# Kernel tuning notes

Measured on AMD Instinct MI355X. Metric: run time of the kernel, lower is better.

## Reference

```python
import jax, jax.numpy as jnp
import numpy as np

N, T, H, E = 16384, 4, 64, 262144
NEG_SLOPE = 0.2  # LeakyReLU slope for GAT-style attention
LN_EPS = 1e-5


def setup_inputs() -> dict:
    key = jax.random.key(0)
    ks = jax.random.split(key, 24)
    p = {}
    p["pred"] = jax.random.normal(ks[0], (N, T, H), jnp.float32)
    p["ei_structural"] = jax.random.randint(ks[1], (2, E), 0, N, jnp.int32)
    p["ei_functional"] = jax.random.randint(ks[2], (2, E), 0, N, jnp.int32)
    scale = 1.0 / np.sqrt(H)
    i = 3
    for l in range(2):
        for et in ("s", "f"):
            p[f"W{l}{et}"] = (jax.random.normal(ks[i], (H, H), jnp.float32) * scale); i += 1
            p[f"a{l}{et}"] = (jax.random.normal(ks[i], (H,), jnp.float32) * scale); i += 1
        p[f"g{l}"] = jnp.ones((H,), jnp.float32)
        p[f"b{l}"] = jnp.zeros((H,), jnp.float32)
    return p


def _conv(x, ei, W, a, n_dst):
    """Attention-based ST graph conv, temporal_kernel_size=1 (per-step)."""
    h = jnp.einsum('nth,hd->ntd', x, W)          # [N,T,H] linear transform
    src, dst = ei[0], ei[1]
    he = h[src]                                   # [E,T,H] gather per edge
    logits = jax.nn.leaky_relu(jnp.einsum('eth,h->et', he, a), NEG_SLOPE)
    m = jax.ops.segment_max(logits, dst, num_segments=n_dst)     # [N,T]
    ex = jnp.exp(logits - m[dst])                 # stable softmax over incoming edges
    den = jax.ops.segment_sum(ex, dst, num_segments=n_dst)
    alpha = ex / den[dst]                         # [E,T]
    return jax.ops.segment_sum(alpha[..., None] * he, dst, num_segments=n_dst)


def _ln(x, g, b):
    mu = x.mean(-1, keepdims=True)
    v = x.var(-1, keepdims=True)
    return (x - mu) * jax.lax.rsqrt(v + LN_EPS) * g + b


def reference(pred, ei_structural, ei_functional,
              W0s, a0s, W0f, a0f, g0, b0,
              W1s, a1s, W1f, a1f, g1, b1):
    x = pred
    layers = ((W0s, a0s, W0f, a0f, g0, b0), (W1s, a1s, W1f, a1f, g1, b1))
    for (Ws, av, Wf, af, g, b) in layers:
        ms = _conv(x, ei_structural, Ws, av, N)
        mf = _conv(x, ei_functional, Wf, af, N)
        # sum(messages)/len(messages), residual, LayerNorm over H (dropout=identity in eval)
        x = _ln(x + 0.5 * (ms + mf), g, b)
    return x
```

## Files before the change

kernel.cpp:

```cpp
#include <hip/hip_runtime.h>
#include <hip/hip_bf16.h>

#define NN 16384
#define TT 4
#define HH 64
#define NT (NN * TT)
#define NEG_SLOPE 0.2f
#define LN_EPS 1e-5f

typedef __attribute__((ext_vector_type(8))) short short8;
typedef __attribute__((ext_vector_type(4))) float f32x4;

__device__ __forceinline__ float bf2f(unsigned short u) {
    return __uint_as_float((unsigned)u << 16);
}
__device__ __forceinline__ unsigned short f2bf(float f) {
    unsigned u = __float_as_uint(f);
    return (unsigned short)((u + 0x7FFF + ((u >> 16) & 1)) >> 16);
}


__global__ void zero_kernel(int* __restrict__ a, int n) {
    int i = blockIdx.x * blockDim.x + threadIdx.x;
    if (i < n) a[i] = 0;
}

__global__ void hist2_kernel(const int* __restrict__ dst_s, const int* __restrict__ dst_f,
                             int* __restrict__ cnt2, int E) {
    int e = blockIdx.x * blockDim.x + threadIdx.x;
    if (e < E) {
        atomicAdd(&cnt2[dst_s[e]], 1);
    } else {
        e -= E;
        if (e < E) atomicAdd(&cnt2[NN + dst_f[e]], 1);
    }
}

__global__ __launch_bounds__(256) void scanA_kernel(const int* __restrict__ cnt2,
                                                    int* __restrict__ partial) {
    __shared__ int wsum[4];
    const int lane = threadIdx.x & 63;
    const int wv = threadIdx.x >> 6;
    int v = cnt2[blockIdx.x * 256 + threadIdx.x];
#pragma unroll
    for (int off = 32; off > 0; off >>= 1) v += __shfl_xor(v, off, 64);
    if (lane == 0) wsum[wv] = v;
    __syncthreads();
    if (threadIdx.x == 0)
        partial[blockIdx.x] = wsum[0] + wsum[1] + wsum[2] + wsum[3];
}

__global__ __launch_bounds__(128) void scanB_kernel(int* __restrict__ partial) {
    const int lane = threadIdx.x & 63;
    int v = partial[threadIdx.x];
    int inc = v;
#pragma unroll
    for (int off = 1; off < 64; off <<= 1) {
        int t = __shfl_up(inc, off, 64);
        if (lane >= off) inc += t;
    }
    partial[threadIdx.x] = inc - v;
}

__global__ __launch_bounds__(256) void scanC_kernel(const int* __restrict__ cnt2,
                                                    const int* __restrict__ partial,
                                                    int* __restrict__ rp2,
                                                    int* __restrict__ cur2) {
    __shared__ int wsum[4];
    const int lane = threadIdx.x & 63;
    const int wv = threadIdx.x >> 6;
    const int gidx = blockIdx.x * 256 + threadIdx.x;
    const int set = gidx >> 14;
    const int i = gidx & (NN - 1);
    int v = cnt2[gidx];
    int inc = v;
#pragma unroll
    for (int off = 1; off < 64; off <<= 1) {
        int t = __shfl_up(inc, off, 64);
        if (lane >= off) inc += t;
    }
    if (lane == 63) wsum[wv] = inc;
    __syncthreads();
    int wbase = 0;
#pragma unroll
    for (int w = 0; w < 4; w++)
        if (w < wv) wbase += wsum[w];
    int excl = (inc - v) + wbase + partial[blockIdx.x];
    int* rp = rp2 + set * (NN + 1);
    rp[i] = excl;
    cur2[gidx] = excl;
    if (i == NN - 1) rp[NN] = excl + v;
}

__global__ void scatter2_kernel(const int* __restrict__ ei_s, const int* __restrict__ ei_f,
                                int* __restrict__ cur2, int* __restrict__ col2, int E) {
    int e = blockIdx.x * blockDim.x + threadIdx.x;
    if (e < E) {
        int d = ei_s[E + e];
        int pos = atomicAdd(&cur2[d], 1);
        col2[pos] = ei_s[e];
    } else {
        e -= E;
        if (e < E) {
            int d = ei_f[E + e];
            int pos = atomicAdd(&cur2[NN + d], 1);
            col2[E + pos] = ei_f[e];
        }
    }
}


__global__ __launch_bounds__(256) void transform2_kernel(
    const float4* __restrict__ x4,
    const float* __restrict__ Ws, const float* __restrict__ as_,
    const float* __restrict__ Wf, const float* __restrict__ af,
    unsigned short* __restrict__ h_s, float* __restrict__ sc_s,
    unsigned short* __restrict__ h_f, float* __restrict__ sc_f) {
    const int lane = threadIdx.x & 63;
    const int wv = threadIdx.x >> 6;
    const int m = lane & 15;
    const int quad = lane >> 4;

    short8 Bs[4][2], Bf[4][2];
#pragma unroll
    for (int c = 0; c < 4; c++) {
#pragma unroll
        for (int ks = 0; ks < 2; ks++) {
#pragma unroll
            for (int j = 0; j < 8; j++) {
                int k = ks * 32 + quad * 8 + j;
                int n = c * 16 + m;
                Bs[c][ks][j] = (short)f2bf(Ws[k * 64 + n]);
                Bf[c][ks][j] = (short)f2bf(Wf[k * 64 + n]);
            }
        }
    }
    float a_s[4], a_f[4];
#pragma unroll
    for (int c = 0; c < 4; c++) { a_s[c] = as_[c * 16 + m]; a_f[c] = af[c * 16 + m]; }

    const int rowbase = blockIdx.x * 128 + wv * 32;
#pragma unroll
    for (int rt = 0; rt < 2; rt++) {
        const int row0 = rowbase + rt * 16;
        const long xbase = (long)(row0 + m) * 16 + quad * 2;
        float4 xa = x4[xbase];
        float4 xb = x4[xbase + 1];
        float4 xc = x4[xbase + 8];
        float4 xd = x4[xbase + 9];
        short8 A0, A1;
        A0[0] = (short)f2bf(xa.x); A0[1] = (short)f2bf(xa.y);
        A0[2] = (short)f2bf(xa.z); A0[3] = (short)f2bf(xa.w);
        A0[4] = (short)f2bf(xb.x); A0[5] = (short)f2bf(xb.y);
        A0[6] = (short)f2bf(xb.z); A0[7] = (short)f2bf(xb.w);
        A1[0] = (short)f2bf(xc.x); A1[1] = (short)f2bf(xc.y);
        A1[2] = (short)f2bf(xc.z); A1[3] = (short)f2bf(xc.w);
        A1[4] = (short)f2bf(xd.x); A1[5] = (short)f2bf(xd.y);
        A1[6] = (short)f2bf(xd.z); A1[7] = (short)f2bf(xd.w);

        f32x4 accs[4], accf[4];
#pragma unroll
        for (int c = 0; c < 4; c++) {
            accs[c] = (f32x4){0.f, 0.f, 0.f, 0.f};
            accf[c] = (f32x4){0.f, 0.f, 0.f, 0.f};
        }
#pragma unroll
        for (int c = 0; c < 4; c++) {
            accs[c] = __builtin_amdgcn_mfma_f32_16x16x32_bf16(A0, Bs[c][0], accs[c], 0, 0, 0);
            accs[c] = __builtin_amdgcn_mfma_f32_16x16x32_bf16(A1, Bs[c][1], accs[c], 0, 0, 0);
            accf[c] = __builtin_amdgcn_mfma_f32_16x16x32_bf16(A0, Bf[c][0], accf[c], 0, 0, 0);
            accf[c] = __builtin_amdgcn_mfma_f32_16x16x32_bf16(A1, Bf[c][1], accf[c], 0, 0, 0);
        }
#pragma unroll
        for (int reg = 0; reg < 4; reg++) {
            const int row = row0 + quad * 4 + reg;
            float ps = 0.f, pf = 0.f;
#pragma unroll
            for (int c = 0; c < 4; c++) {
                h_s[(long)row * 64 + c * 16 + m] = f2bf(accs[c][reg]);
                h_f[(long)row * 64 + c * 16 + m] = f2bf(accf[c][reg]);
                ps = fmaf(accs[c][reg], a_s[c], ps);
                pf = fmaf(accf[c][reg], a_f[c], pf);
            }
#pragma unroll
            for (int off = 1; off < 16; off <<= 1) {
                ps += __shfl_xor(ps, off, 64);
                pf += __shfl_xor(pf, off, 64);
            }
            if (m == 0) {
                sc_s[row] = (ps > 0.f) ? ps : NEG_SLOPE * ps;
                sc_f[row] = (pf > 0.f) ? pf : NEG_SLOPE * pf;
            }
        }
    }
}


__device__ __forceinline__ void agg_set(const ushort4* __restrict__ h4,
                                        const float* __restrict__ sc,
                                        const int* __restrict__ rp,
                                        const int* __restrict__ col,
                                        int n, int t, int lane, float4& msg) {
    const int beg = rp[n], end = rp[n + 1];
    float den = 0.f;
    float ax = 0.f, ay = 0.f, az = 0.f, aw = 0.f;
    int j = beg;
    for (; j + 8 <= end; j += 8) {
        int s[8];
        float l[8];
        ushort4 hh[8];
#pragma unroll
        for (int u = 0; u < 8; u++) s[u] = col[j + u];
#pragma unroll
        for (int u = 0; u < 8; u++) l[u] = sc[s[u] * 4 + t];
#pragma unroll
        for (int u = 0; u < 8; u++) hh[u] = h4[s[u] * 64 + lane];
#pragma unroll
        for (int u = 0; u < 8; u++) {
            float e = __expf(l[u]);
            den += e;
            ax = fmaf(e, bf2f(hh[u].x), ax);
            ay = fmaf(e, bf2f(hh[u].y), ay);
            az = fmaf(e, bf2f(hh[u].z), az);
            aw = fmaf(e, bf2f(hh[u].w), aw);
        }
    }
    for (; j + 4 <= end; j += 4) {
        int s[4];
        float l[4];
        ushort4 hh[4];
#pragma unroll
        for (int u = 0; u < 4; u++) s[u] = col[j + u];
#pragma unroll
        for (int u = 0; u < 4; u++) l[u] = sc[s[u] * 4 + t];
#pragma unroll
        for (int u = 0; u < 4; u++) hh[u] = h4[s[u] * 64 + lane];
#pragma unroll
        for (int u = 0; u < 4; u++) {
            float e = __expf(l[u]);
            den += e;
            ax = fmaf(e, bf2f(hh[u].x), ax);
            ay = fmaf(e, bf2f(hh[u].y), ay);
            az = fmaf(e, bf2f(hh[u].z), az);
            aw = fmaf(e, bf2f(hh[u].w), aw);
        }
    }
    for (; j < end; j++) {
        int s0 = col[j];
        float l0 = sc[s0 * 4 + t];
        ushort4 h0 = h4[s0 * 64 + lane];
        float e0 = __expf(l0);
        den += e0;
        ax = fmaf(e0, bf2f(h0.x), ax);
        ay = fmaf(e0, bf2f(h0.y), ay);
        az = fmaf(e0, bf2f(h0.z), az);
        aw = fmaf(e0, bf2f(h0.w), aw);
    }
    if (end > beg) {
        float r = 1.f / den;
        msg.x = ax * r; msg.y = ay * r; msg.z = az * r; msg.w = aw * r;
    } else {
        msg.x = msg.y = msg.z = msg.w = 0.f;
    }
}

__global__ __launch_bounds__(256) void aggregate_kernel(
    const float4* __restrict__ x4,
    const ushort4* __restrict__ hs4, const float* __restrict__ scs,
    const int* __restrict__ rps, const int* __restrict__ cols,
    const ushort4* __restrict__ hf4, const float* __restrict__ scf,
    const int* __restrict__ rpf, const int* __restrict__ colf,
    const float4* __restrict__ g4, const float4* __restrict__ b4,
    float4* __restrict__ out4) {
    __shared__ float4 msgF[2][64];
    const int wv = threadIdx.x >> 6;
    const int lane = threadIdx.x & 63;
    const int slot = wv >> 1;
    const int set = wv & 1;
    const int n = blockIdx.x * 2 + slot;
    const int t = lane >> 4;
    const int ci = lane & 15;

    float4 msg;
    if (set == 0) {
        agg_set(hs4, scs, rps, cols, n, t, lane, msg);
    } else {
        agg_set(hf4, scf, rpf, colf, n, t, lane, msg);
        msgF[slot][lane] = msg;
    }
    __syncthreads();
    if (set == 1) return;

    float4 mf = msgF[slot][lane];
    float4 xv = x4[n * 64 + lane];

    float v0 = xv.x + 0.5f * (msg.x + mf.x);
    float v1 = xv.y + 0.5f * (msg.y + mf.y);
    float v2 = xv.z + 0.5f * (msg.z + mf.z);
    float v3 = xv.w + 0.5f * (msg.w + mf.w);

    float sum = (v0 + v1) + (v2 + v3);
#pragma unroll
    for (int off = 1; off < 16; off <<= 1) sum += __shfl_xor(sum, off, 64);
    float mu = sum * (1.f / 64.f);
    float d0 = v0 - mu, d1 = v1 - mu, d2 = v2 - mu, d3 = v3 - mu;
    float var = (d0 * d0 + d1 * d1) + (d2 * d2 + d3 * d3);
#pragma unroll
    for (int off = 1; off < 16; off <<= 1) var += __shfl_xor(var, off, 64);
    var *= (1.f / 64.f);
    float inv = rsqrtf(var + LN_EPS);
    float4 gv = g4[ci], bv = b4[ci];
    float4 o;
    o.x = d0 * inv * gv.x + bv.x;
    o.y = d1 * inv * gv.y + bv.y;
    o.z = d2 * inv * gv.z + bv.z;
    o.w = d3 * inv * gv.w + bv.w;
    out4[n * 64 + lane] = o;
}


extern "C" void kernel_launch(void* const* d_in, const int* in_sizes, int n_in,
                              void* d_out, int out_size, void* d_ws, size_t ws_size,
                              hipStream_t stream) {
    const float* pred = (const float*)d_in[0];
    const int* ei_s = (const int*)d_in[1];
    const int* ei_f = (const int*)d_in[2];
    const float* W0s = (const float*)d_in[3];
    const float* a0s = (const float*)d_in[4];
    const float* W0f = (const float*)d_in[5];
    const float* a0f = (const float*)d_in[6];
    const float* g0  = (const float*)d_in[7];
    const float* b0  = (const float*)d_in[8];
    const float* W1s = (const float*)d_in[9];
    const float* a1s = (const float*)d_in[10];
    const float* W1f = (const float*)d_in[11];
    const float* a1f = (const float*)d_in[12];
    const float* g1  = (const float*)d_in[13];
    const float* b1  = (const float*)d_in[14];
    const int E = in_sizes[1] / 2;

    char* ws = (char*)d_ws;
    auto alloc = [&](size_t bytes) {
        char* p = ws;
        ws += (bytes + 255) & ~(size_t)255;
        return p;
    };
    int* cnt2 = (int*)alloc((size_t)2 * NN * sizeof(int));
    int* rp2  = (int*)alloc((size_t)2 * (NN + 1) * sizeof(int));
    int* cur2 = (int*)alloc((size_t)2 * NN * sizeof(int));
    int* col2 = (int*)alloc((size_t)2 * E * sizeof(int));
    int* partial = (int*)alloc(128 * sizeof(int));
    unsigned short* h_s = (unsigned short*)alloc((size_t)NT * HH * sizeof(unsigned short));
    unsigned short* h_f = (unsigned short*)alloc((size_t)NT * HH * sizeof(unsigned short));
    float* sc_s = (float*)alloc((size_t)NT * sizeof(float));
    float* sc_f = (float*)alloc((size_t)NT * sizeof(float));
    float* x_mid = (float*)alloc((size_t)NT * HH * sizeof(float));

    const int* rp_s = rp2;
    const int* rp_f = rp2 + (NN + 1);
    const int* col_s = col2;
    const int* col_f = col2 + E;

    const int EB = (E + 255) / 256;

    zero_kernel<<<(2 * NN) / 256, 256, 0, stream>>>(cnt2, 2 * NN);
    hist2_kernel<<<2 * EB, 256, 0, stream>>>(ei_s + E, ei_f + E, cnt2, E);
    scanA_kernel<<<128, 256, 0, stream>>>(cnt2, partial);
    scanB_kernel<<<1, 128, 0, stream>>>(partial);
    scanC_kernel<<<128, 256, 0, stream>>>(cnt2, partial, rp2, cur2);
    scatter2_kernel<<<2 * EB, 256, 0, stream>>>(ei_s, ei_f, cur2, col2, E);

    transform2_kernel<<<NT / 128, 256, 0, stream>>>(
        (const float4*)pred, W0s, a0s, W0f, a0f, h_s, sc_s, h_f, sc_f);
    aggregate_kernel<<<NN / 2, 256, 0, stream>>>(
        (const float4*)pred, (const ushort4*)h_s, sc_s, rp_s, col_s,
        (const ushort4*)h_f, sc_f, rp_f, col_f,
        (const float4*)g0, (const float4*)b0, (float4*)x_mid);

    transform2_kernel<<<NT / 128, 256, 0, stream>>>(
        (const float4*)x_mid, W1s, a1s, W1f, a1f, h_s, sc_s, h_f, sc_f);
    aggregate_kernel<<<NN / 2, 256, 0, stream>>>(
        (const float4*)x_mid, (const ushort4*)h_s, sc_s, rp_s, col_s,
        (const ushort4*)h_f, sc_f, rp_f, col_f,
        (const float4*)g1, (const float4*)b1, (float4*)d_out);
}
```

Measured before the change: 254.0 us.

## Store h and scores time-major and split aggregation per timestep across lanes

The transform kernel now writes h and attention scores in a [T][N] layout, so each timestep's node features sit in a contiguous per-step table. Aggregation launches one block set per (timestep, half of nodes) and uses the four 16-lane groups of a wave to process four different edges at once, then reduces across groups with shuffles. This is meant to shrink the gathered working set per block to one timestep's slice, which improves cache locality, and to raise memory-level parallelism. In exchange the launch has 4x more blocks, some lanes idle on tail edges, and extra shuffle reductions are needed.

```diff
diff --git a/kernel.cpp b/kernel.cpp
--- a/kernel.cpp
+++ b/kernel.cpp
@@ -174,11 +174,14 @@
 #pragma unroll
         for (int reg = 0; reg < 4; reg++) {
             const int row = row0 + quad * 4 + reg;
+            const int node = row >> 2;
+            const int tt = row & 3;
+            const long hb = ((long)tt * NN + node) * 64;
             float ps = 0.f, pf = 0.f;
 #pragma unroll
             for (int c = 0; c < 4; c++) {
-                h_s[(long)row * 64 + c * 16 + m] = f2bf(accs[c][reg]);
-                h_f[(long)row * 64 + c * 16 + m] = f2bf(accf[c][reg]);
+                h_s[hb + c * 16 + m] = f2bf(accs[c][reg]);
+                h_f[hb + c * 16 + m] = f2bf(accf[c][reg]);
                 ps = fmaf(accs[c][reg], a_s[c], ps);
                 pf = fmaf(accf[c][reg], a_f[c], pf);
             }
@@ -188,81 +191,13 @@
                 pf += __shfl_xor(pf, off, 64);
             }
             if (m == 0) {
-                sc_s[row] = (ps > 0.f) ? ps : NEG_SLOPE * ps;
-                sc_f[row] = (pf > 0.f) ? pf : NEG_SLOPE * pf;
+                sc_s[tt * NN + node] = (ps > 0.f) ? ps : NEG_SLOPE * ps;
+                sc_f[tt * NN + node] = (pf > 0.f) ? pf : NEG_SLOPE * pf;
             }
         }
     }
 }
 
-
-__device__ __forceinline__ void agg_set(const ushort4* __restrict__ h4,
-                                        const float* __restrict__ sc,
-                                        const int* __restrict__ rp,
-                                        const int* __restrict__ col,
-                                        int n, int t, int lane, float4& msg) {
-    const int beg = rp[n], end = rp[n + 1];
-    float den = 0.f;
-    float ax = 0.f, ay = 0.f, az = 0.f, aw = 0.f;
-    int j = beg;
-    for (; j + 8 <= end; j += 8) {
-        int s[8];
-        float l[8];
-        ushort4 hh[8];
-#pragma unroll
-        for (int u = 0; u < 8; u++) s[u] = col[j + u];
-#pragma unroll
-        for (int u = 0; u < 8; u++) l[u] = sc[s[u] * 4 + t];
-#pragma unroll
-        for (int u = 0; u < 8; u++) hh[u] = h4[s[u] * 64 + lane];
-#pragma unroll
-        for (int u = 0; u < 8; u++) {
-            float e = __expf(l[u]);
-            den += e;
-            ax = fmaf(e, bf2f(hh[u].x), ax);
-            ay = fmaf(e, bf2f(hh[u].y), ay);
-            az = fmaf(e, bf2f(hh[u].z), az);
-            aw = fmaf(e, bf2f(hh[u].w), aw);
-        }
-    }
-    for (; j + 4 <= end; j += 4) {
-        int s[4];
-        float l[4];
-        ushort4 hh[4];
-#pragma unroll
-        for (int u = 0; u < 4; u++) s[u] = col[j + u];
-#pragma unroll
-        for (int u = 0; u < 4; u++) l[u] = sc[s[u] * 4 + t];
-#pragma unroll
-        for (int u = 0; u < 4; u++) hh[u] = h4[s[u] * 64 + lane];
-#pragma unroll
-        for (int u = 0; u < 4; u++) {
-            float e = __expf(l[u]);
-            den += e;
-            ax = fmaf(e, bf2f(hh[u].x), ax);
-            ay = fmaf(e, bf2f(hh[u].y), ay);
-            az = fmaf(e, bf2f(hh[u].z), az);
-            aw = fmaf(e, bf2f(hh[u].w), aw);
-        }
-    }
-    for (; j < end; j++) {
-        int s0 = col[j];
-        float l0 = sc[s0 * 4 + t];
-        ushort4 h0 = h4[s0 * 64 + lane];
-        float e0 = __expf(l0);
-        den += e0;
-        ax = fmaf(e0, bf2f(h0.x), ax);
-        ay = fmaf(e0, bf2f(h0.y), ay);
-        az = fmaf(e0, bf2f(h0.z), az);
-        aw = fmaf(e0, bf2f(h0.w), aw);
-    }
-    if (end > beg) {
-        float r = 1.f / den;
-        msg.x = ax * r; msg.y = ay * r; msg.z = az * r; msg.w = aw * r;
-    } else {
-        msg.x = msg.y = msg.z = msg.w = 0.f;
-    }
-}
 
 __global__ __launch_bounds__(256) void aggregate_kernel(
     const float4* __restrict__ x4,
@@ -272,27 +207,64 @@
     const int* __restrict__ rpf, const int* __restrict__ colf,
     const float4* __restrict__ g4, const float4* __restrict__ b4,
     float4* __restrict__ out4) {
-    __shared__ float4 msgF[2][64];
+    __shared__ float4 msgF[2][16];
     const int wv = threadIdx.x >> 6;
     const int lane = threadIdx.x & 63;
     const int slot = wv >> 1;
     const int set = wv & 1;
-    const int n = blockIdx.x * 2 + slot;
-    const int t = lane >> 4;
+    const int r = blockIdx.x & 7;
+    const int t = r >> 1;
+    const int half = r & 1;
+    const int n = half * (NN / 2) + (blockIdx.x >> 3) * 2 + slot;
+    const int u = lane >> 4;
     const int ci = lane & 15;
 
+    const ushort4* h4 = set ? hf4 : hs4;
+    const float* sc = set ? scf : scs;
+    const int* rp = set ? rpf : rps;
+    const int* col = set ? colf : cols;
+
+    const float* sct = sc + t * NN;
+    const ushort4* ht = h4 + (size_t)t * NN * 16;
+
+    const int beg = rp[n], end = rp[n + 1];
+    float den = 0.f;
+    float4 acc = {0.f, 0.f, 0.f, 0.f};
+    for (int j = beg; j < end; j += 4) {
+        const int je = j + u;
+        const bool ok = (je < end);
+        int s0 = ok ? col[je] : col[beg];
+        float l = ok ? sct[s0] : -INFINITY;
+        ushort4 hh = ht[s0 * 16 + ci];
+        float e = __expf(l);
+        den += e;
+        acc.x = fmaf(e, bf2f(hh.x), acc.x);
+        acc.y = fmaf(e, bf2f(hh.y), acc.y);
+        acc.z = fmaf(e, bf2f(hh.z), acc.z);
+        acc.w = fmaf(e, bf2f(hh.w), acc.w);
+    }
+#pragma unroll
+    for (int off = 16; off < 64; off <<= 1) {
+        den += __shfl_xor(den, off, 64);
+        acc.x += __shfl_xor(acc.x, off, 64);
+        acc.y += __shfl_xor(acc.y, off, 64);
+        acc.z += __shfl_xor(acc.z, off, 64);
+        acc.w += __shfl_xor(acc.w, off, 64);
+    }
     float4 msg;
-    if (set == 0) {
-        agg_set(hs4, scs, rps, cols, n, t, lane, msg);
+    if (end > beg) {
+        float rd = 1.f / den;
+        msg.x = acc.x * rd; msg.y = acc.y * rd; msg.z = acc.z * rd; msg.w = acc.w * rd;
     } else {
-        agg_set(hf4, scf, rpf, colf, n, t, lane, msg);
-        msgF[slot][lane] = msg;
-    }
+        msg.x = msg.y = msg.z = msg.w = 0.f;
+    }
+
+    if (set == 1 && u == 0) msgF[slot][ci] = msg;
     __syncthreads();
     if (set == 1) return;
 
-    float4 mf = msgF[slot][lane];
-    float4 xv = x4[n * 64 + lane];
+    float4 mf = msgF[slot][ci];
+    float4 xv = x4[(n * 4 + t) * 16 + ci];
 
     float v0 = xv.x + 0.5f * (msg.x + mf.x);
     float v1 = xv.y + 0.5f * (msg.y + mf.y);
@@ -315,7 +287,7 @@
     o.y = d1 * inv * gv.y + bv.y;
     o.z = d2 * inv * gv.z + bv.z;
     o.w = d3 * inv * gv.w + bv.w;
-    out4[n * 64 + lane] = o;
+    if (u == 0) out4[(n * 4 + t) * 16 + ci] = o;
 }
 
 
@@ -372,14 +344,14 @@
 
     transform2_kernel<<<NT / 128, 256, 0, stream>>>(
         (const float4*)pred, W0s, a0s, W0f, a0f, h_s, sc_s, h_f, sc_f);
-    aggregate_kernel<<<NN / 2, 256, 0, stream>>>(
+    aggregate_kernel<<<2 * NN, 256, 0, stream>>>(
         (const float4*)pred, (const ushort4*)h_s, sc_s, rp_s, col_s,
         (const ushort4*)h_f, sc_f, rp_f, col_f,
         (const float4*)g0, (const float4*)b0, (float4*)x_mid);
 
     transform2_kernel<<<NT / 128, 256, 0, stream>>>(
         (const float4*)x_mid, W1s, a1s, W1f, a1f, h_s, sc_s, h_f, sc_f);
-    aggregate_kernel<<<NN / 2, 256, 0, stream>>>(
+    aggregate_kernel<<<2 * NN, 256, 0, stream>>>(
         (const float4*)x_mid, (const ushort4*)h_s, sc_s, rp_s, col_s,
         (const ushort4*)h_f, sc_f, rp_f, col_f,
         (const float4*)g1, (const float4*)b1, (float4*)d_out);
```

Measured after the change: 366.9 us. 1.44x slower.
